# Kernel optimization log

Hardware: AMD Instinct MI355X
Metric: run time of the kernel (lower is better)

## Reference

```python
import jax, jax.numpy as jnp
import numpy as np

N_WIN = 7
NUM_HEADS = 8
DIM = 256
QK = 256
TOPK = 4
MLP_HID = 4 * DIM
SCALE = QK ** -0.5  # used for both region routing and pixel attention (qk_scale=None)


def _layernorm(x, g, b, eps=1e-6):
    mu = jnp.mean(x, axis=-1, keepdims=True)
    var = jnp.mean(jnp.square(x - mu), axis=-1, keepdims=True)
    return (x - mu) * jax.lax.rsqrt(var + eps) * g + b


def _dwconv(x, w, b):
    # x: NHWC, w: (5,5,1,C) depthwise kernel (torch Conv2d groups=C, padding=2)
    y = jax.lax.conv_general_dilated(
        x, w, window_strides=(1, 1), padding='SAME',
        feature_group_count=x.shape[-1],
        dimension_numbers=('NHWC', 'HWIO', 'NHWC'))
    return y + b


def _bra(x, qkv_w, qkv_b, lepe_w, lepe_b, wo_w, wo_b):
    # BiLevelRoutingAttention, NHWC in/out
    N, H, W, C = x.shape
    j = i = N_WIN
    h, w = H // j, W // i
    p2, w2, m = j * i, h * w, NUM_HEADS
    dq, dv = QK // m, C // m
    # window partition: (N, p2, h, w, C)
    xw = x.reshape(N, j, h, i, w, C).transpose(0, 1, 3, 2, 4, 5).reshape(N, p2, h, w, C)
    qkv = xw @ qkv_w + qkv_b
    q = qkv[..., :QK]            # (N,p2,h,w,QK)
    kv = qkv[..., QK:]           # (N,p2,h,w,QK+C)
    q_pix = q.reshape(N, p2, w2, QK)
    kv_pix = kv.reshape(N, p2, w2, QK + C)
    q_win = jnp.mean(q, axis=(2, 3))                    # (N,p2,QK)
    k_win = jnp.mean(kv[..., :QK], axis=(2, 3))         # (N,p2,QK)
    # LePE: depthwise conv on V in full-image layout
    v_img = kv[..., QK:].reshape(N, j, i, h, w, C).transpose(0, 1, 3, 2, 4, 5).reshape(N, H, W, C)
    lepe = _dwconv(v_img, lepe_w, lepe_b)
    # region-to-region routing, top-k window selection
    logit = jnp.einsum('npc,nqc->npq', q_win * SCALE, k_win)    # (N,p2,p2)
    _, r_idx = jax.lax.top_k(logit, TOPK)                       # (N,p2,TOPK)
    # gather KV of selected windows: (N,p2,TOPK,w2,QK+C)
    kv_sel = kv_pix[jnp.arange(N)[:, None, None], r_idx]
    k_sel = kv_sel[..., :QK].reshape(N, p2, TOPK * w2, m, dq).transpose(0, 1, 3, 2, 4)  # (N,p2,m,kw2,dq)
    v_sel = kv_sel[..., QK:].reshape(N, p2, TOPK * w2, m, dv).transpose(0, 1, 3, 2, 4)  # (N,p2,m,kw2,dv)
    q_h = q_pix.reshape(N, p2, w2, m, dq).transpose(0, 1, 3, 2, 4)                      # (N,p2,m,w2,dq)
    aw = jnp.einsum('npmqd,npmkd->npmqk', q_h * SCALE, k_sel)
    aw = jax.nn.softmax(aw, axis=-1)
    out = jnp.einsum('npmqk,npmkd->npmqd', aw, v_sel)           # (N,p2,m,w2,dv)
    out = out.transpose(0, 1, 3, 2, 4).reshape(N, j, i, h, w, C)
    out = out.transpose(0, 1, 3, 2, 4, 5).reshape(N, H, W, C)
    out = out + lepe
    return out @ wo_w + wo_b


def setup_inputs() -> dict:
    key = jax.random.key(0)
    ks = jax.random.split(key, 8)
    s = 0.02
    return {
        'x': jax.random.normal(ks[0], (8, 56, 56, DIM), dtype=jnp.float32),
        'ln1_g': jnp.ones((DIM,), jnp.float32),
        'ln1_b': jnp.zeros((DIM,), jnp.float32),
        'qkv_w': jax.random.normal(ks[1], (DIM, 2 * QK + DIM), jnp.float32) * s,
        'qkv_b': jnp.zeros((2 * QK + DIM,), jnp.float32),
        'lepe_w': jax.random.normal(ks[2], (5, 5, 1, DIM), jnp.float32) * s,
        'lepe_b': jnp.zeros((DIM,), jnp.float32),
        'wo_w': jax.random.normal(ks[3], (DIM, DIM), jnp.float32) * s,
        'wo_b': jnp.zeros((DIM,), jnp.float32),
        'ln2_g': jnp.ones((DIM,), jnp.float32),
        'ln2_b': jnp.zeros((DIM,), jnp.float32),
        'mlp_w1': jax.random.normal(ks[4], (DIM, MLP_HID), jnp.float32) * s,
        'mlp_b1': jnp.zeros((MLP_HID,), jnp.float32),
        'mlp_w2': jax.random.normal(ks[5], (MLP_HID, DIM), jnp.float32) * s,
        'mlp_b2': jnp.zeros((DIM,), jnp.float32),
    }


def reference(x, ln1_g, ln1_b, qkv_w, qkv_b, lepe_w, lepe_b, wo_w, wo_b,
              ln2_g, ln2_b, mlp_w1, mlp_b1, mlp_w2, mlp_b2):
    x = x + _bra(_layernorm(x, ln1_g, ln1_b), qkv_w, qkv_b, lepe_w, lepe_b, wo_w, wo_b)
    h = _layernorm(x, ln2_g, ln2_b)
    h = jax.nn.gelu(h @ mlp_w1 + mlp_b1, approximate=False) @ mlp_w2 + mlp_b2
    return x + h
```

## Files before the change

### kernel.cpp

```cpp
#include <hip/hip_runtime.h>
#include <hip/hip_bf16.h>

#define NIMG 8
#define HW 56
#define CDIM 256
#define TOK (NIMG*HW*HW)
#define NWIN 49
#define NPW (NIMG*NWIN)
#define ATT_SCALE 0.0625f

typedef __attribute__((ext_vector_type(8))) short short8;
typedef __attribute__((ext_vector_type(4))) short short4v;
typedef __attribute__((ext_vector_type(4))) float f32x4;

static const size_t OFF_WQKV  = 0;
static const size_t OFF_WWO   = 393216;
static const size_t OFF_W1    = 524288;
static const size_t OFF_W2    = 1048576;
static const size_t OFF_XLN   = 1572864;
static const size_t OFF_QKV   = 14417920;
static const size_t OFF_QKWIN = 52953088;
static const size_t OFF_RIDX  = 53755904;
static const size_t OFF_ATTN  = 53762176;
static const size_t OFF_HMID  = OFF_XLN;

__device__ __forceinline__ float gelu_exact(float v) {
    return 0.5f * v * (1.f + erff(v * 0.70710678118654752f));
}
__device__ __forceinline__ short f2bs(float x) {
    __hip_bfloat16 h = __float2bfloat16(x);
    return *(short*)&h;
}
__device__ __forceinline__ float bs2f(short s) {
    return __uint_as_float(((unsigned)(unsigned short)s) << 16);
}
__device__ __forceinline__ void gld16(const short* g, short* l) {
    __builtin_amdgcn_global_load_lds(
        (const __attribute__((address_space(1))) void*)g,
        (__attribute__((address_space(3))) void*)l, 16, 0, 0);
}

__global__ __launch_bounds__(256) void transpose_cast4_k(const float* __restrict__ s0,
                                                         const float* __restrict__ s1,
                                                         const float* __restrict__ s2,
                                                         const float* __restrict__ s3,
                                                         __hip_bfloat16* __restrict__ d0,
                                                         __hip_bfloat16* __restrict__ d1,
                                                         __hip_bfloat16* __restrict__ d2,
                                                         __hip_bfloat16* __restrict__ d3) {
    int b = blockIdx.x;
    const float* src; __hip_bfloat16* dst; int K, N, l;
    if (b < 192)      { src = s0; dst = d0; K = 256;  N = 768;  l = b; }
    else if (b < 256) { src = s1; dst = d1; K = 256;  N = 256;  l = b - 192; }
    else if (b < 512) { src = s2; dst = d2; K = 256;  N = 1024; l = b - 256; }
    else              { src = s3; dst = d3; K = 1024; N = 256;  l = b - 512; }
    int nx = N / 32;
    int n0 = (l % nx) * 32, k0 = (l / nx) * 32;
    __shared__ float t[32][33];
    int tx = threadIdx.x & 31, ty = threadIdx.x >> 5;
    #pragma unroll
    for (int i = 0; i < 32; i += 8)
        t[ty + i][tx] = src[(size_t)(k0 + ty + i) * N + n0 + tx];
    __syncthreads();
    #pragma unroll
    for (int i = 0; i < 32; i += 8)
        dst[(size_t)(n0 + ty + i) * K + k0 + tx] = __float2bfloat16(t[tx][ty + i]);
}

__global__ __launch_bounds__(256) void ln_bf_k(const float* __restrict__ in,
                                               const float* __restrict__ g,
                                               const float* __restrict__ b,
                                               short* __restrict__ out, int remap) {
    int t = blockIdx.x * 4 + (threadIdx.x >> 6);
    int lane = threadIdx.x & 63;
    float4 v = *(const float4*)(in + (size_t)t * 256 + lane * 4);
    float s = v.x + v.y + v.z + v.w;
    float s2 = v.x * v.x + v.y * v.y + v.z * v.z + v.w * v.w;
    #pragma unroll
    for (int o = 32; o > 0; o >>= 1) {
        s  += __shfl_xor(s, o);
        s2 += __shfl_xor(s2, o);
    }
    float mu = s * (1.f / 256.f);
    float rstd = rsqrtf(s2 * (1.f / 256.f) - mu * mu + 1e-6f);
    float4 gv = *(const float4*)(g + lane * 4);
    float4 bv = *(const float4*)(b + lane * 4);
    short4v o;
    o[0] = f2bs((v.x - mu) * rstd * gv.x + bv.x);
    o[1] = f2bs((v.y - mu) * rstd * gv.y + bv.y);
    o[2] = f2bs((v.z - mu) * rstd * gv.z + bv.z);
    o[3] = f2bs((v.w - mu) * rstd * gv.w + bv.w);
    size_t tb;
    if (remap) {
        int n = t / 3136, rem = t % 3136, y = rem / 56, x = rem % 56;
        int p = (y >> 3) * 7 + (x >> 3);
        int si = (y & 7) * 8 + (x & 7);
        tb = (size_t)(n * 49 + p) * 64 + si;
    } else {
        tb = (size_t)t;
    }
    *(short4v*)(out + tb * 256 + lane * 4) = o;
}

template<int MODE>
__global__ __launch_bounds__(256) void gemm64(const short* __restrict__ A,
                                              const short* __restrict__ Bt,
                                              const float* __restrict__ bias,
                                              const float* __restrict__ res,
                                              void* Cv, int M, int N, int K) {
    const int bn = blockIdx.x * 128;
    const int bm = blockIdx.y * 64;
    const int tid = threadIdx.x;
    const int wave = tid >> 6, lane = tid & 63;
    const int l15 = lane & 15, quad = lane >> 4;
    const int wm = (wave & 1) * 32, wn = (wave >> 1) * 64;

    __shared__ __align__(16) short smem[6144];
    short* As = smem;
    short* Bs = smem + 2048;

    f32x4 acc[2][4];
    #pragma unroll
    for (int i = 0; i < 2; ++i)
        #pragma unroll
        for (int j = 0; j < 4; ++j) acc[i][j] = (f32x4){0.f, 0.f, 0.f, 0.f};

    const int crow = lane >> 2;
    const int ckq = (lane & 3) * 8;
    const short* ga  = A  + (size_t)(bm + wave * 16 + crow) * K + ckq;
    const short* gb0 = Bt + (size_t)(bn + wave * 16 + crow) * K + ckq;
    const short* gb1 = gb0 + (size_t)64 * K;
    short* la  = As + wave * 512;
    short* lb0 = Bs + wave * 512;
    short* lb1 = Bs + 2048 + wave * 512;

    for (int k0 = 0; k0 < K; k0 += 32) {
        gld16(ga + k0, la);
        gld16(gb0 + k0, lb0);
        gld16(gb1 + k0, lb1);
        __syncthreads();
        short8 af[2], bfr[4];
        #pragma unroll
        for (int i = 0; i < 2; ++i)
            af[i] = *(const short8*)&As[(wm + i * 16 + l15) * 32 + quad * 8];
        #pragma unroll
        for (int j = 0; j < 4; ++j)
            bfr[j] = *(const short8*)&Bs[(wn + j * 16 + l15) * 32 + quad * 8];
        #pragma unroll
        for (int i = 0; i < 2; ++i)
            #pragma unroll
            for (int j = 0; j < 4; ++j)
                acc[i][j] = __builtin_amdgcn_mfma_f32_16x16x32_bf16(af[i], bfr[j], acc[i][j], 0, 0, 0);
        __syncthreads();
    }

    if (MODE == 1) {
        #pragma unroll
        for (int i = 0; i < 2; ++i) {
            int row = bm + wm + i * 16 + quad * 4;
            #pragma unroll
            for (int j = 0; j < 4; ++j) {
                int col = bn + wn + j * 16 + l15;
                float bia = bias[col];
                #pragma unroll
                for (int r = 0; r < 4; ++r) {
                    size_t idx = (size_t)(row + r) * N + col;
                    ((float*)Cv)[idx] = acc[i][j][r] + bia + res[idx];
                }
            }
        }
    } else {
        float biasv[4];
        #pragma unroll
        for (int j = 0; j < 4; ++j) biasv[j] = bias[bn + wn + j * 16 + l15];
        short* ep = &smem[wave * 1280];
        short* outp = (short*)Cv;
        #pragma unroll
        for (int p = 0; p < 2; ++p) {
            #pragma unroll
            for (int i = 0; i < 2; ++i)
                #pragma unroll
                for (int jj = 0; jj < 2; ++jj) {
                    int j = p * 2 + jj;
                    #pragma unroll
                    for (int r = 0; r < 4; ++r) {
                        float v = acc[i][j][r] + biasv[j];
                        if (MODE == 2) v = gelu_exact(v);
                        ep[(i * 16 + quad * 4 + r) * 40 + jj * 16 + l15] = f2bs(v);
                    }
                }
            __builtin_amdgcn_s_waitcnt(0);
            int c = lane & 3;
            #pragma unroll
            for (int rr = 0; rr < 2; ++rr) {
                int row = rr * 16 + (lane >> 2);
                short8 v = *(const short8*)&ep[row * 40 + c * 8];
                *(short8*)&outp[(size_t)(bm + wm + row) * N + bn + wn + p * 32 + c * 8] = v;
            }
            __builtin_amdgcn_s_waitcnt(0);
        }
    }
}

__global__ __launch_bounds__(256) void win_means_k(const short* __restrict__ qkv,
                                                   float* __restrict__ qkwin) {
    int w = blockIdx.x;
    int cg = (threadIdx.x & 63) * 8;
    int sp = threadIdx.x >> 6;
    float s[8] = {0.f, 0.f, 0.f, 0.f, 0.f, 0.f, 0.f, 0.f};
    const short* base = qkv + (size_t)w * 64 * 768 + cg;
    for (int si = sp; si < 64; si += 4) {
        short8 v = *(const short8*)(base + (size_t)si * 768);
        #pragma unroll
        for (int i = 0; i < 8; ++i) s[i] += bs2f(v[i]);
    }
    __shared__ float red[4][512];
    #pragma unroll
    for (int i = 0; i < 8; ++i) red[sp][cg + i] = s[i];
    __syncthreads();
    for (int c = threadIdx.x; c < 512; c += 256) {
        float t = red[0][c] + red[1][c] + red[2][c] + red[3][c];
        qkwin[(size_t)w * 512 + c] = t * (1.f / 64.f);
    }
}

__global__ __launch_bounds__(64) void route_k(const float* __restrict__ qkwin,
                                              int* __restrict__ ridx) {
    int w = blockIdx.x;
    int n = w / 49;
    int tid = threadIdx.x;
    __shared__ float qv[256];
    __shared__ float lg[49];
    for (int i = tid; i < 256; i += 64) qv[i] = qkwin[(size_t)w * 512 + i] * ATT_SCALE;
    __syncthreads();
    if (tid < 49) {
        const float* kp = qkwin + (size_t)(n * 49 + tid) * 512 + 256;
        float d = 0.f;
        for (int cc = 0; cc < 256; ++cc) d += qv[cc] * kp[cc];
        lg[tid] = d;
    }
    __syncthreads();
    if (tid == 0) {
        #pragma unroll
        for (int t = 0; t < 4; ++t) {
            float best = -1e30f; int bi = 0;
            for (int j = 0; j < 49; ++j)
                if (lg[j] > best) { best = lg[j]; bi = j; }
            lg[bi] = -1e30f;
            ridx[w * 4 + t] = bi;
        }
    }
}

__global__ __launch_bounds__(256) void attn_mfma_k(const short* __restrict__ qkv,
                                                   const int* __restrict__ ridx,
                                                   short* __restrict__ attn) {
    const int blk = blockIdx.x;
    const int w = blk >> 3, h = blk & 7;
    const int n = w / 49;
    const int tid = threadIdx.x;
    const int wave = tid >> 6, lane = tid & 63;
    const int l15 = lane & 15, quad = lane >> 4;

    __shared__ __align__(16) short Ks[256 * 40];
    __shared__ __align__(16) short Vt[32 * 264];
    __shared__ __align__(16) short Ps[4 * 16 * 264];
    __shared__ int rs4[4];
    if (tid < 4) rs4[tid] = ridx[w * 4 + tid];
    __syncthreads();

    {
        int s = tid >> 2, kq = (tid & 3) * 8;
        #pragma unroll
        for (int u = 0; u < 4; ++u) {
            int key = u * 64 + s;
            const short* src = qkv + ((size_t)(n * 49 + rs4[u]) * 64 + s) * 768 + 256 + h * 32 + kq;
            *(short8*)&Ks[key * 40 + kq] = *(const short8*)src;
        }
    }
    {
        int key = tid;
        int t = key >> 6, s = key & 63;
        const short* src = qkv + ((size_t)(n * 49 + rs4[t]) * 64 + s) * 768 + 512 + h * 32;
        #pragma unroll
        for (int u = 0; u < 4; ++u) {
            short8 v = *(const short8*)(src + u * 8);
            #pragma unroll
            for (int i = 0; i < 8; ++i)
                Vt[(u * 8 + i) * 264 + key] = v[i];
        }
    }
    __syncthreads();

    const short* qp = qkv + ((size_t)w * 64 + wave * 16 + l15) * 768 + h * 32 + quad * 8;
    short8 qf = *(const short8*)qp;

    f32x4 st[16];
    #pragma unroll
    for (int j = 0; j < 16; ++j) {
        short8 kf = *(const short8*)&Ks[(j * 16 + l15) * 40 + quad * 8];
        st[j] = __builtin_amdgcn_mfma_f32_16x16x32_bf16(qf, kf, (f32x4){0.f, 0.f, 0.f, 0.f}, 0, 0, 0);
    }

    float lr[4];
    short* pw = &Ps[wave * 16 * 264];
    #pragma unroll
    for (int r = 0; r < 4; ++r) {
        float mx = -1e30f;
        #pragma unroll
        for (int j = 0; j < 16; ++j) mx = fmaxf(mx, st[j][r]);
        #pragma unroll
        for (int off = 1; off < 16; off <<= 1) mx = fmaxf(mx, __shfl_xor(mx, off));
        float sum = 0.f;
        #pragma unroll
        for (int j = 0; j < 16; ++j) {
            float p = __expf((st[j][r] - mx) * ATT_SCALE);
            sum += p;
            pw[(quad * 4 + r) * 264 + j * 16 + l15] = f2bs(p);
        }
        #pragma unroll
        for (int off = 1; off < 16; off <<= 1) sum += __shfl_xor(sum, off);
        lr[r] = sum;
    }
    __syncthreads();

    f32x4 oc[2] = {(f32x4){0.f,0.f,0.f,0.f}, (f32x4){0.f,0.f,0.f,0.f}};
    #pragma unroll
    for (int kk = 0; kk < 8; ++kk) {
        short8 pf = *(const short8*)&pw[l15 * 264 + kk * 32 + quad * 8];
        #pragma unroll
        for (int jj = 0; jj < 2; ++jj) {
            short8 vf = *(const short8*)&Vt[(jj * 16 + l15) * 264 + kk * 32 + quad * 8];
            oc[jj] = __builtin_amdgcn_mfma_f32_16x16x32_bf16(pf, vf, oc[jj], 0, 0, 0);
        }
    }

    short* op = attn + ((size_t)w * 64 + wave * 16) * 256 + h * 32;
    #pragma unroll
    for (int jj = 0; jj < 2; ++jj)
        #pragma unroll
        for (int r = 0; r < 4; ++r)
            op[(size_t)(quad * 4 + r) * 256 + jj * 16 + l15] = f2bs(oc[jj][r] / lr[r]);
}

__global__ __launch_bounds__(256) void lepe_k(const short* __restrict__ qkv,
                                              const short* __restrict__ attn,
                                              const float* __restrict__ lw,
                                              const float* __restrict__ lb,
                                              short* __restrict__ ywo) {
    int t = blockIdx.x * 8 + (threadIdx.x >> 5);
    int c0 = (threadIdx.x & 31) * 8;
    int n = t / 3136, rem = t % 3136, y = rem / 56, x = rem % 56;
    float sum[8];
    {
        float4 b0 = *(const float4*)(lb + c0), b1 = *(const float4*)(lb + c0 + 4);
        sum[0] = b0.x; sum[1] = b0.y; sum[2] = b0.z; sum[3] = b0.w;
        sum[4] = b1.x; sum[5] = b1.y; sum[6] = b1.z; sum[7] = b1.w;
    }
    #pragma unroll
    for (int ky = 0; ky < 5; ++ky) {
        int yy = y + ky - 2;
        if ((unsigned)yy >= 56u) continue;
        #pragma unroll
        for (int kx = 0; kx < 5; ++kx) {
            int xx = x + kx - 2;
            if ((unsigned)xx >= 56u) continue;
            int p = (yy >> 3) * 7 + (xx >> 3);
            int si = (yy & 7) * 8 + (xx & 7);
            short8 v = *(const short8*)(qkv + ((size_t)(n * 49 + p) * 64 + si) * 768 + 512 + c0);
            const float* wp = lw + (ky * 5 + kx) * 256 + c0;
            float4 w0 = *(const float4*)wp, w1 = *(const float4*)(wp + 4);
            sum[0] += bs2f(v[0]) * w0.x; sum[1] += bs2f(v[1]) * w0.y;
            sum[2] += bs2f(v[2]) * w0.z; sum[3] += bs2f(v[3]) * w0.w;
            sum[4] += bs2f(v[4]) * w1.x; sum[5] += bs2f(v[5]) * w1.y;
            sum[6] += bs2f(v[6]) * w1.z; sum[7] += bs2f(v[7]) * w1.w;
        }
    }
    int p0 = (y >> 3) * 7 + (x >> 3);
    int s0 = (y & 7) * 8 + (x & 7);
    short8 a = *(const short8*)(attn + ((size_t)(n * 49 + p0) * 64 + s0) * 256 + c0);
    short8 o;
    #pragma unroll
    for (int i = 0; i < 8; ++i) o[i] = f2bs(sum[i] + bs2f(a[i]));
    *(short8*)(ywo + (size_t)t * 256 + c0) = o;
}

extern "C" void kernel_launch(void* const* d_in, const int* in_sizes, int n_in,
                              void* d_out, int out_size, void* d_ws, size_t ws_size,
                              hipStream_t stream) {
    const float* x      = (const float*)d_in[0];
    const float* ln1_g  = (const float*)d_in[1];
    const float* ln1_b  = (const float*)d_in[2];
    const float* qkv_w  = (const float*)d_in[3];
    const float* qkv_b  = (const float*)d_in[4];
    const float* lepe_w = (const float*)d_in[5];
    const float* lepe_b = (const float*)d_in[6];
    const float* wo_w   = (const float*)d_in[7];
    const float* wo_b   = (const float*)d_in[8];
    const float* ln2_g  = (const float*)d_in[9];
    const float* ln2_b  = (const float*)d_in[10];
    const float* mlp_w1 = (const float*)d_in[11];
    const float* mlp_b1 = (const float*)d_in[12];
    const float* mlp_w2 = (const float*)d_in[13];
    const float* mlp_b2 = (const float*)d_in[14];
    float* out = (float*)d_out;

    char* ws = (char*)d_ws;
    __hip_bfloat16* wqkvT = (__hip_bfloat16*)(ws + OFF_WQKV);
    __hip_bfloat16* wwoT  = (__hip_bfloat16*)(ws + OFF_WWO);
    __hip_bfloat16* w1T   = (__hip_bfloat16*)(ws + OFF_W1);
    __hip_bfloat16* w2T   = (__hip_bfloat16*)(ws + OFF_W2);
    short* xln   = (short*)(ws + OFF_XLN);
    short* qkvb  = (short*)(ws + OFF_QKV);
    float* qkwin = (float*)(ws + OFF_QKWIN);
    int*   ridx  = (int*)(ws + OFF_RIDX);
    short* attnb = (short*)(ws + OFF_ATTN);
    short* ywo   = (short*)(ws + OFF_XLN);
    short* h2    = (short*)(ws + OFF_ATTN);
    short* hmid  = (short*)(ws + OFF_HMID);

    transpose_cast4_k<<<768, 256, 0, stream>>>(qkv_w, wo_w, mlp_w1, mlp_w2,
                                               wqkvT, wwoT, w1T, w2T);
    ln_bf_k<<<TOK/4, 256, 0, stream>>>(x, ln1_g, ln1_b, xln, 1);
    gemm64<0><<<dim3(6, 392), 256, 0, stream>>>(xln, (const short*)wqkvT,
                                                qkv_b, nullptr, qkvb, TOK, 768, 256);
    win_means_k<<<NPW, 256, 0, stream>>>(qkvb, qkwin);
    route_k<<<NPW, 64, 0, stream>>>(qkwin, ridx);
    attn_mfma_k<<<NPW * 8, 256, 0, stream>>>(qkvb, ridx, attnb);
    lepe_k<<<TOK/8, 256, 0, stream>>>(qkvb, attnb, lepe_w, lepe_b, ywo);
    gemm64<1><<<dim3(2, 392), 256, 0, stream>>>(ywo, (const short*)wwoT,
                                                wo_b, x, out, TOK, 256, 256);
    ln_bf_k<<<TOK/4, 256, 0, stream>>>(out, ln2_g, ln2_b, h2, 0);
    gemm64<2><<<dim3(8, 392), 256, 0, stream>>>(h2, (const short*)w1T,
                                                mlp_b1, nullptr, hmid, TOK, 1024, 256);
    gemm64<1><<<dim3(2, 392), 256, 0, stream>>>(hmid, (const short*)w2T,
                                                mlp_b2, out, out, TOK, 256, 1024);
}
```

Baseline: 313.1 us.

## Transpose attention MFMA operands so each lane owns a query row and alias LDS

Swaps the MFMA operand order in the attention kernel so each lane holds one query row's scores. Row max and sum then need only two cross-lane shuffles, and P and the output are written as packed 4-element vectors instead of scalar stores. The V transpose now packs two keys per 32-bit LDS store, and the K and P buffers share LDS to shrink the footprint and allow more resident blocks. This adds an extra barrier before P overwrites K and relies on a manual waitcnt for intra-wave LDS visibility.

```diff
diff --git a/kernel.cpp b/kernel.cpp
--- a/kernel.cpp
+++ b/kernel.cpp
@@ -262,9 +262,10 @@
     const int wave = tid >> 6, lane = tid & 63;
     const int l15 = lane & 15, quad = lane >> 4;
 
-    __shared__ __align__(16) short Ks[256 * 40];
-    __shared__ __align__(16) short Vt[32 * 264];
-    __shared__ __align__(16) short Ps[4 * 16 * 264];
+    __shared__ __align__(16) short smem[25344];
+    short* Vt = smem;
+    short* Ks = smem + 8448;
+    short* Ps = smem + 8448;
     __shared__ int rs4[4];
     if (tid < 4) rs4[tid] = ridx[w * 4 + tid];
     __syncthreads();
@@ -279,15 +280,19 @@
         }
     }
     {
-        int key = tid;
-        int t = key >> 6, s = key & 63;
-        const short* src = qkv + ((size_t)(n * 49 + rs4[t]) * 64 + s) * 768 + 512 + h * 32;
-        #pragma unroll
-        for (int u = 0; u < 4; ++u) {
-            short8 v = *(const short8*)(src + u * 8);
-            #pragma unroll
-            for (int i = 0; i < 8; ++i)
-                Vt[(u * 8 + i) * 264 + key] = v[i];
+        int kp = tid & 127, dh = tid >> 7;
+        int k0 = kp * 2;
+        int t = k0 >> 6, s = k0 & 63;
+        const short* src0 = qkv + ((size_t)(n * 49 + rs4[t]) * 64 + s) * 768 + 512 + h * 32 + dh * 16;
+        const short* src1 = src0 + 768;
+        short8 a0 = *(const short8*)src0, a1 = *(const short8*)(src0 + 8);
+        short8 b0 = *(const short8*)src1, b1 = *(const short8*)(src1 + 8);
+        #pragma unroll
+        for (int d = 0; d < 8; ++d) {
+            *(unsigned*)&Vt[(dh * 16 + d) * 264 + k0] =
+                (unsigned)(unsigned short)a0[d] | ((unsigned)(unsigned short)b0[d] << 16);
+            *(unsigned*)&Vt[(dh * 16 + 8 + d) * 264 + k0] =
+                (unsigned)(unsigned short)a1[d] | ((unsigned)(unsigned short)b1[d] << 16);
         }
     }
     __syncthreads();
@@ -299,30 +304,36 @@
     #pragma unroll
     for (int j = 0; j < 16; ++j) {
         short8 kf = *(const short8*)&Ks[(j * 16 + l15) * 40 + quad * 8];
-        st[j] = __builtin_amdgcn_mfma_f32_16x16x32_bf16(qf, kf, (f32x4){0.f, 0.f, 0.f, 0.f}, 0, 0, 0);
-    }
-
-    float lr[4];
+        st[j] = __builtin_amdgcn_mfma_f32_16x16x32_bf16(kf, qf, (f32x4){0.f, 0.f, 0.f, 0.f}, 0, 0, 0);
+    }
+
+    float mx = -1e30f;
+    #pragma unroll
+    for (int j = 0; j < 16; ++j)
+        #pragma unroll
+        for (int r = 0; r < 4; ++r) mx = fmaxf(mx, st[j][r]);
+    mx = fmaxf(mx, __shfl_xor(mx, 16));
+    mx = fmaxf(mx, __shfl_xor(mx, 32));
+
+    __syncthreads();
+
     short* pw = &Ps[wave * 16 * 264];
-    #pragma unroll
-    for (int r = 0; r < 4; ++r) {
-        float mx = -1e30f;
-        #pragma unroll
-        for (int j = 0; j < 16; ++j) mx = fmaxf(mx, st[j][r]);
-        #pragma unroll
-        for (int off = 1; off < 16; off <<= 1) mx = fmaxf(mx, __shfl_xor(mx, off));
-        float sum = 0.f;
-        #pragma unroll
-        for (int j = 0; j < 16; ++j) {
+    float sum = 0.f;
+    #pragma unroll
+    for (int j = 0; j < 16; ++j) {
+        short4v pv;
+        #pragma unroll
+        for (int r = 0; r < 4; ++r) {
             float p = __expf((st[j][r] - mx) * ATT_SCALE);
             sum += p;
-            pw[(quad * 4 + r) * 264 + j * 16 + l15] = f2bs(p);
-        }
-        #pragma unroll
-        for (int off = 1; off < 16; off <<= 1) sum += __shfl_xor(sum, off);
-        lr[r] = sum;
-    }
-    __syncthreads();
+            pv[r] = f2bs(p);
+        }
+        *(short4v*)&pw[l15 * 264 + j * 16 + quad * 4] = pv;
+    }
+    sum += __shfl_xor(sum, 16);
+    sum += __shfl_xor(sum, 32);
+    float inv = 1.f / sum;
+    __builtin_amdgcn_s_waitcnt(0);
 
     f32x4 oc[2] = {(f32x4){0.f,0.f,0.f,0.f}, (f32x4){0.f,0.f,0.f,0.f}};
     #pragma unroll
@@ -331,16 +342,18 @@
         #pragma unroll
         for (int jj = 0; jj < 2; ++jj) {
             short8 vf = *(const short8*)&Vt[(jj * 16 + l15) * 264 + kk * 32 + quad * 8];
-            oc[jj] = __builtin_amdgcn_mfma_f32_16x16x32_bf16(pf, vf, oc[jj], 0, 0, 0);
-        }
-    }
-
-    short* op = attn + ((size_t)w * 64 + wave * 16) * 256 + h * 32;
-    #pragma unroll
-    for (int jj = 0; jj < 2; ++jj)
-        #pragma unroll
-        for (int r = 0; r < 4; ++r)
-            op[(size_t)(quad * 4 + r) * 256 + jj * 16 + l15] = f2bs(oc[jj][r] / lr[r]);
+            oc[jj] = __builtin_amdgcn_mfma_f32_16x16x32_bf16(vf, pf, oc[jj], 0, 0, 0);
+        }
+    }
+
+    short* op = attn + ((size_t)w * 64 + wave * 16 + l15) * 256 + h * 32;
+    #pragma unroll
+    for (int jj = 0; jj < 2; ++jj) {
+        short4v o4;
+        #pragma unroll
+        for (int r = 0; r < 4; ++r) o4[r] = f2bs(oc[jj][r] * inv);
+        *(short4v*)&op[jj * 16 + quad * 4] = o4;
+    }
 }
 
 __global__ __launch_bounds__(256) void lepe_k(const short* __restrict__ qkv,
```

Result: faster. 299.8 us (-4.2%).
